# Optimization experiments

Hardware: AMD Instinct MI355X
Metric: run time of the kernel (lower is better)

Reference implementation:

```python
import jax, jax.numpy as jnp
import numpy as np

N_LINK, N_FLOW, N_PATH = 2000, 30000, 50000
E1, E2 = 120000, 120000
HID, H, D = 256, 4, 256  # hidden_size, num_heads, per-head out_feats (= hidden)
OUT = 2
NEG_SLOPE = 0.2


def gat_conv(z_src, z_dst, src, dst, attn_l, attn_r, n_dst, ee=None):
    """Edge-GAT aggregation. z_src:[Ns,H,D], z_dst:[Nd,H,D], ee:[E,H] or None -> [Nd,H,D]."""
    el = (z_src * attn_l).sum(-1)  # [Ns,H]
    er = (z_dst * attn_r).sum(-1)  # [Nd,H]
    e = el[src] + er[dst]          # [E,H]
    if ee is not None:
        e = e + ee
    e = jax.nn.leaky_relu(e, NEG_SLOPE)
    m = jax.ops.segment_max(e, dst, num_segments=n_dst)
    m = jnp.where(jnp.isfinite(m), m, 0.0)  # empty segments -> -inf
    a = jnp.exp(e - m[dst])
    denom = jax.ops.segment_sum(a, dst, num_segments=n_dst)
    alpha = a / jnp.maximum(denom[dst], 1e-9)
    return jax.ops.segment_sum(alpha[:, :, None] * z_src[src], dst, num_segments=n_dst)


def setup_inputs() -> dict:
    key = jax.random.key(0)
    ks = jax.random.split(key, 32)
    s = jnp.float32(0.05)
    lin = lambda k, i, o: (jax.random.normal(k, (i, o), jnp.float32) * s)
    vec = lambda k, h, d: (jax.random.normal(k, (h, d), jnp.float32) * s)
    inp = {
        'x_link': jax.random.normal(ks[0], (N_LINK, 8), jnp.float32),
        'x_flow': jax.random.normal(ks[1], (N_FLOW, 16), jnp.float32),
        'x_path': jax.random.normal(ks[2], (N_PATH, 8), jnp.float32),
        'e2p_feature': jax.random.uniform(ks[3], (E1, 1), jnp.float32),
        'Wp_link': lin(ks[8], 8, HID), 'bp_link': jnp.zeros((HID,), jnp.float32),
        'Wp_flow': lin(ks[9], 16, HID), 'bp_flow': jnp.zeros((HID,), jnp.float32),
        'Wp_path': lin(ks[10], 8, HID), 'bp_path': jnp.zeros((HID,), jnp.float32),
        'fc_src1': lin(ks[11], HID, H * D), 'fc_dst1': lin(ks[12], HID, H * D),
        'fc_e1': lin(ks[13], 1, H * D),
        'attn_l1': vec(ks[14], H, D), 'attn_r1': vec(ks[15], H, D), 'attn_e1': vec(ks[16], H, D),
        'res_W1': lin(ks[17], HID, HID),
        'fc_src2': lin(ks[18], HID, H * D), 'fc_dst2': lin(ks[19], HID, H * D),
        'attn_l2': vec(ks[20], H, D), 'attn_r2': vec(ks[21], H, D),
        'res_W2': lin(ks[22], HID, HID),
        'W1': lin(ks[23], 3 * HID, HID), 'b1': jnp.zeros((HID,), jnp.float32),
        'W2': lin(ks[24], HID, OUT), 'b2': jnp.zeros((OUT,), jnp.float32),
        'src1': jax.random.randint(ks[4], (E1,), 0, N_LINK),
        'dst1': jax.random.randint(ks[5], (E1,), 0, N_PATH),
        'src2': jax.random.randint(ks[6], (E2,), 0, N_FLOW),
        'dst2': jax.random.randint(ks[7], (E2,), 0, N_PATH),
    }
    return inp


def reference(x_link, x_flow, x_path, e2p_feature,
              Wp_link, bp_link, Wp_flow, bp_flow, Wp_path, bp_path,
              fc_src1, fc_dst1, fc_e1, attn_l1, attn_r1, attn_e1, res_W1,
              fc_src2, fc_dst2, attn_l2, attn_r2, res_W2,
              W1, b1, W2, b2, src1, dst1, src2, dst2):
    # per-node-type projection + relu
    h_link = jax.nn.relu(x_link @ Wp_link + bp_link)
    h_flow = jax.nn.relu(x_flow @ Wp_flow + bp_flow)
    h_path = jax.nn.relu(x_path @ Wp_path + bp_path)

    # conv_1: link -> path (edge features e2p_feature, edge_feats=1)
    z_s = (h_link @ fc_src1).reshape(-1, H, D)
    z_d = (h_path @ fc_dst1).reshape(-1, H, D)
    ee = ((e2p_feature @ fc_e1).reshape(-1, H, D) * attn_e1).sum(-1)  # [E1,H]
    agg = gat_conv(z_s, z_d, src1, dst1, attn_l1, attn_r1, N_PATH, ee)
    h_path = jax.nn.relu(agg.mean(axis=1) + h_path @ res_W1)
    x_res1 = h_path

    # conv_2: flow -> path (no edge features)
    z_s = (h_flow @ fc_src2).reshape(-1, H, D)
    z_d = (h_path @ fc_dst2).reshape(-1, H, D)
    agg = gat_conv(z_s, z_d, src2, dst2, attn_l2, attn_r2, N_PATH)
    h_path = jax.nn.relu(agg.mean(axis=1) + h_path @ res_W2)
    x_res2 = h_path

    # linear decoder (dropout = identity in eval)
    x = jnp.concatenate([h_path, x_res1, x_res2], axis=-1)  # [N_PATH, 3*HID]
    x = jax.nn.relu(x @ W1 + b1)
    return x @ W2 + b2  # [N_PATH, OUT]
```

## Files before the change

kernel.cpp:

```cpp
#include <hip/hip_runtime.h>
#include <math.h>

typedef unsigned int uint;
typedef unsigned short ushort;

#define HIDF 256
#define HD4 1024
#define NHEAD 4
#define N_LINK 2000
#define N_FLOW 30000
#define N_PATH 50000
#define NEDGE 120000
#define N_CVT 26
#define NB_SCAN ((N_PATH + 1023) / 1024)

__device__ inline float bf_lo(uint u) { return __uint_as_float(u << 16); }
__device__ inline float bf_hi(uint u) { return __uint_as_float(u & 0xffff0000u); }
__device__ inline float ldb(const ushort* p) { return __uint_as_float(((uint)*p) << 16); }
__device__ inline ushort f2b(float f) {
    uint x = __float_as_uint(f);
    return (ushort)((x + 0x7fffu + ((x >> 16) & 1u)) >> 16);
}

typedef __attribute__((ext_vector_type(8))) short bf16x8;
typedef __attribute__((ext_vector_type(4))) float f32x4;

__global__ void detect_dtype(const ushort* __restrict__ probe, int* __restrict__ flag) {
    int lane = threadIdx.x;
    uint u = probe[lane * 2];
    int e = (u >> 7) & 0xFF;
    bool sane = (u != 0u) && (e <= 0x4F);
    unsigned long long m = __ballot(sane);
    if (lane == 0) *flag = (__popcll(m) >= 48) ? 1 : 0;
}

struct CvtArgs {
    const void* src[N_CVT];
    int off[N_CVT];
    int sz[N_CVT];
};

__global__ __launch_bounds__(256) void convert_inputs(CvtArgs a, ushort* __restrict__ dst,
                                                      const int* __restrict__ flag) {
    int i = blockIdx.y;
    int idx = blockIdx.x * 256 + threadIdx.x;
    if (idx >= a.sz[i]) return;
    ushort v;
    if (*flag) v = ((const ushort*)a.src[i])[idx];
    else       v = f2b(((const float*)a.src[i])[idx]);
    dst[a.off[i] + idx] = v;
}

__global__ void sentinel_fill(void* out, int n, float val, const int* flag) {
    int i = blockIdx.x * 256 + threadIdx.x;
    if (i >= n) return;
    if (*flag) ((ushort*)out)[i] = f2b(val);
    else       ((float*)out)[i] = val;
}

__global__ void prep_small(const ushort* __restrict__ fc_src1, const ushort* __restrict__ attn_l1,
                           const ushort* __restrict__ fc_dst1, const ushort* __restrict__ attn_r1,
                           const ushort* __restrict__ fc_src2, const ushort* __restrict__ attn_l2,
                           const ushort* __restrict__ fc_dst2, const ushort* __restrict__ attn_r2,
                           const ushort* __restrict__ fc_e1,   const ushort* __restrict__ attn_e1,
                           float* wl1, float* wr1, float* wl2, float* wr2, float* c1) {
    int h = blockIdx.x;
    int k = threadIdx.x;
    float a = 0.f, b = 0.f, c = 0.f, d = 0.f;
    for (int dd = 0; dd < HIDF; ++dd) {
        int fi = k * HD4 + h * HIDF + dd;
        int ai = h * HIDF + dd;
        a += ldb(fc_src1 + fi) * ldb(attn_l1 + ai);
        b += ldb(fc_dst1 + fi) * ldb(attn_r1 + ai);
        c += ldb(fc_src2 + fi) * ldb(attn_l2 + ai);
        d += ldb(fc_dst2 + fi) * ldb(attn_r2 + ai);
    }
    wl1[k * NHEAD + h] = a;
    wr1[k * NHEAD + h] = b;
    wl2[k * NHEAD + h] = c;
    wr2[k * NHEAD + h] = d;
    if (k == 0) {
        float s = 0.f;
        for (int dd = 0; dd < HIDF; ++dd) s += ldb(fc_e1 + h * HIDF + dd) * ldb(attn_e1 + h * HIDF + dd);
        c1[h] = s;
    }
}

struct TJobs {
    const ushort* s1[6];
    const ushort* s2[6];
    ushort* d[6];
    int K[6];
    int N[6];
};

__global__ __launch_bounds__(256) void transpose_batch(TJobs tj) {
    int j = blockIdx.y;
    int K = tj.K[j], N = tj.N[j];
    int tilesx = N >> 5;
    if ((int)blockIdx.x >= tilesx * (K >> 5)) return;
    int n0 = (blockIdx.x % tilesx) * 32, k0 = (blockIdx.x / tilesx) * 32;
    const ushort* s1 = tj.s1[j];
    const ushort* s2 = tj.s2[j];
    ushort* dst = tj.d[j];
    __shared__ ushort tile[32][33];
    int jj = threadIdx.x & 31, i0 = threadIdx.x >> 5;
    for (int i = i0; i < 32; i += 8) {
        size_t idx = (size_t)(k0 + i) * N + n0 + jj;
        float v = ldb(s1 + idx);
        if (s2) v += ldb(s2 + idx);
        tile[i][jj] = f2b(v);
    }
    __syncthreads();
    for (int i = i0; i < 32; i += 8) dst[(size_t)(n0 + i) * K + k0 + jj] = tile[jj][i];
}

template <int K>
__device__ inline void proj_body(const ushort* __restrict__ X, const ushort* __restrict__ W,
                                 const ushort* __restrict__ bias, ushort* __restrict__ Y, int i) {
    int j = threadIdx.x;
    float x[K];
#pragma unroll
    for (int k = 0; k < K; ++k) x[k] = ldb(X + i * K + k);
    float s = ldb(bias + j);
#pragma unroll
    for (int k = 0; k < K; ++k) s += x[k] * ldb(W + k * HIDF + j);
    Y[(size_t)i * HIDF + j] = f2b(fmaxf(s, 0.f));
}

__global__ __launch_bounds__(256) void proj_all(const ushort* X0, const ushort* W0, const ushort* b0, ushort* Y0,
                                                const ushort* X1, const ushort* W1, const ushort* b1, ushort* Y1,
                                                const ushort* X2, const ushort* W2, const ushort* b2, ushort* Y2) {
    int b = blockIdx.x;
    if (b < N_LINK) proj_body<8>(X0, W0, b0, Y0, b);
    else if (b < N_LINK + N_FLOW) proj_body<16>(X1, W1, b1, Y1, b - N_LINK);
    else proj_body<8>(X2, W2, b2, Y2, b - N_LINK - N_FLOW);
}

#define GTM 64
#define GTN 128
#define GTK 32
#define GPAD 40

#define LOAD_TILE(t)                                                          \
    {                                                                         \
        const ushort* A;                                                      \
        const ushort* BT;                                                     \
        int K, k0;                                                            \
        if ((t) < nt1) { A = A1; BT = B1T; K = K1; k0 = (t)*GTK; }            \
        else           { A = A2; BT = B2T; K = K2; k0 = ((t)-nt1) * GTK; }    \
        av = (bm + ar < M) ? *(const uint4*)(A + (size_t)(bm + ar) * K + k0 + aq * 8) : z4; \
        bv0 = *(const uint4*)(BT + (size_t)(bn + ar) * K + k0 + aq * 8);      \
        bv1 = *(const uint4*)(BT + (size_t)(bn + ar + 64) * K + k0 + aq * 8); \
    }

#define STORE_TILE(b)                                                         \
    {                                                                         \
        *(uint4*)&As[b][ar][aq * 8] = av;                                     \
        *(uint4*)&Bs[b][ar][aq * 8] = bv0;                                    \
        *(uint4*)&Bs[b][ar + 64][aq * 8] = bv1;                               \
    }

__global__ __launch_bounds__(256) void gemm_mfma(const ushort* __restrict__ A1, const ushort* __restrict__ B1T, int K1,
                                                 const ushort* __restrict__ A2, const ushort* __restrict__ B2T, int K2,
                                                 const ushort* __restrict__ Dadd, const ushort* __restrict__ bias,
                                                 int do_relu, ushort* __restrict__ C, int M, int N) {
    __shared__ __align__(16) ushort As[2][GTM][GPAD];
    __shared__ __align__(16) ushort Bs[2][GTN][GPAD];

    int tid = threadIdx.x;
    int lane = tid & 63, wave = tid >> 6;
    int quad = lane >> 4, l16 = lane & 15;
    int wn = wave * 32;
    int bm = blockIdx.y * GTM, bn = blockIdx.x * GTN;

    f32x4 acc[4][2];
    f32x4 zf = {0.f, 0.f, 0.f, 0.f};
#pragma unroll
    for (int i = 0; i < 4; ++i) {
        acc[i][0] = zf;
        acc[i][1] = zf;
    }

    int ar = tid >> 2, aq = tid & 3;
    uint4 av, bv0, bv1;
    uint4 z4 = {0, 0, 0, 0};

    int nt1 = K1 / GTK;
    int ntot = nt1 + K2 / GTK;

    LOAD_TILE(0);
    STORE_TILE(0);
    __syncthreads();

    for (int t = 0; t < ntot; ++t) {
        int cur = t & 1, nxt = cur ^ 1;
        if (t + 1 < ntot) LOAD_TILE(t + 1);

        bf16x8 af[4], bf[2];
#pragma unroll
        for (int mt = 0; mt < 4; ++mt) af[mt] = *(const bf16x8*)&As[cur][mt * 16 + l16][quad * 8];
#pragma unroll
        for (int ct = 0; ct < 2; ++ct) bf[ct] = *(const bf16x8*)&Bs[cur][wn + ct * 16 + l16][quad * 8];
#pragma unroll
        for (int mt = 0; mt < 4; ++mt)
#pragma unroll
            for (int ct = 0; ct < 2; ++ct)
                acc[mt][ct] = __builtin_amdgcn_mfma_f32_16x16x32_bf16(af[mt], bf[ct], acc[mt][ct], 0, 0, 0);

        if (t + 1 < ntot) STORE_TILE(nxt);
        __syncthreads();
    }

#pragma unroll
    for (int mt = 0; mt < 4; ++mt) {
#pragma unroll
        for (int ct = 0; ct < 2; ++ct) {
            int col = bn + wn + ct * 16 + l16;
#pragma unroll
            for (int rg = 0; rg < 4; ++rg) {
                int row = bm + mt * 16 + quad * 4 + rg;
                if (row >= M) continue;
                float v = acc[mt][ct][rg];
                if (Dadd) v += ldb(Dadd + (size_t)row * N + col);
                if (bias) v += ldb(bias + col);
                if (do_relu) v = fmaxf(v, 0.f);
                C[(size_t)row * N + col] = f2b(v);
            }
        }
    }
}

__device__ inline void rowdot4_body(const ushort* __restrict__ X, const float* __restrict__ W,
                                    float* __restrict__ Y, int row) {
    int lane = threadIdx.x & 63;
    uint2 xu = *(const uint2*)(X + (size_t)row * HIDF + lane * 4);
    float x[4] = {bf_lo(xu.x), bf_hi(xu.x), bf_lo(xu.y), bf_hi(xu.y)};
    float p0 = 0.f, p1 = 0.f, p2 = 0.f, p3 = 0.f;
#pragma unroll
    for (int i = 0; i < 4; ++i) {
        int k = lane * 4 + i;
        p0 += x[i] * W[k * 4 + 0];
        p1 += x[i] * W[k * 4 + 1];
        p2 += x[i] * W[k * 4 + 2];
        p3 += x[i] * W[k * 4 + 3];
    }
#pragma unroll
    for (int off = 32; off >= 1; off >>= 1) {
        p0 += __shfl_down(p0, off, 64);
        p1 += __shfl_down(p1, off, 64);
        p2 += __shfl_down(p2, off, 64);
        p3 += __shfl_down(p3, off, 64);
    }
    if (lane == 0) {
        Y[(size_t)row * 4 + 0] = p0;
        Y[(size_t)row * 4 + 1] = p1;
        Y[(size_t)row * 4 + 2] = p2;
        Y[(size_t)row * 4 + 3] = p3;
    }
}

__global__ __launch_bounds__(256) void rowdot_pair(const ushort* XA, const float* WA, float* YA, int MA,
                                                   const ushort* XB, const float* WB, float* YB, int MB) {
    int nblkA = (MA + 3) / 4;
    int wv = threadIdx.x >> 6;
    if ((int)blockIdx.x < nblkA) {
        int row = blockIdx.x * 4 + wv;
        if (row < MA) rowdot4_body(XA, WA, YA, row);
    } else {
        int row = (blockIdx.x - nblkA) * 4 + wv;
        if (row < MB) rowdot4_body(XB, WB, YB, row);
    }
}

__global__ __launch_bounds__(256) void rowdot_out(const ushort* __restrict__ X, const ushort* __restrict__ W2,
                                                  const ushort* __restrict__ b2, void* __restrict__ Y, int M,
                                                  const int* __restrict__ flag) {
    int wv = threadIdx.x >> 6, lane = threadIdx.x & 63;
    int row = blockIdx.x * 4 + wv;
    if (row >= M) return;
    uint2 xu = *(const uint2*)(X + (size_t)row * HIDF + lane * 4);
    float x[4] = {bf_lo(xu.x), bf_hi(xu.x), bf_lo(xu.y), bf_hi(xu.y)};
    float p0 = 0.f, p1 = 0.f;
#pragma unroll
    for (int i = 0; i < 4; ++i) {
        int k = lane * 4 + i;
        p0 += x[i] * ldb(W2 + k * 2 + 0);
        p1 += x[i] * ldb(W2 + k * 2 + 1);
    }
#pragma unroll
    for (int off = 32; off >= 1; off >>= 1) {
        p0 += __shfl_down(p0, off, 64);
        p1 += __shfl_down(p1, off, 64);
    }
    if (lane == 0) {
        float v0 = p0 + ldb(b2 + 0);
        float v1 = p1 + ldb(b2 + 1);
        if (*flag) {
            ((ushort*)Y)[(size_t)row * 2 + 0] = f2b(v0);
            ((ushort*)Y)[(size_t)row * 2 + 1] = f2b(v1);
        } else {
            ((float*)Y)[(size_t)row * 2 + 0] = v0;
            ((float*)Y)[(size_t)row * 2 + 1] = v1;
        }
    }
}

__global__ void edge_pass_a(const int* __restrict__ src, const int* __restrict__ dst,
                            const float* __restrict__ el, const float* __restrict__ er,
                            const ushort* __restrict__ e2p, const float* __restrict__ c1,
                            float* __restrict__ abuf, float* __restrict__ denom,
                            int* __restrict__ cnt, int E) {
    int e = blockIdx.x * 256 + threadIdx.x;
    if (e >= E) return;
    int s = src[e], d = dst[e];
    float ev = e2p ? ldb(e2p + e) : 0.f;
#pragma unroll
    for (int h = 0; h < NHEAD; ++h) {
        float v = el[s * NHEAD + h] + er[d * NHEAD + h];
        if (e2p) v += c1[h] * ev;
        v = v > 0.f ? v : 0.2f * v;
        float a = __expf(v);
        abuf[e * NHEAD + h] = a;
        atomicAdd(&denom[d * NHEAD + h], a);
    }
    atomicAdd(&cnt[d], 1);
}

__global__ __launch_bounds__(1024) void scan_block(const int* __restrict__ cnt, int* __restrict__ starts,
                                                   int* __restrict__ bsum, int n) {
    __shared__ int sd[1024];
    int t = threadIdx.x, i = blockIdx.x * 1024 + t;
    int x = (i < n) ? cnt[i] : 0;
    sd[t] = x;
    __syncthreads();
    for (int o = 1; o < 1024; o <<= 1) {
        int v = (t >= o) ? sd[t - o] : 0;
        __syncthreads();
        sd[t] += v;
        __syncthreads();
    }
    if (i < n) starts[i] = sd[t] - x;
    if (t == 1023) bsum[blockIdx.x] = sd[t];
}

__global__ void scan_part(int* __restrict__ bsum, int nb) {
    int b = threadIdx.x;
    int x = (b < nb) ? bsum[b] : 0;
    int orig = x;
    for (int o = 1; o < 64; o <<= 1) {
        int v = __shfl_up(x, o, 64);
        if (b >= o) x += v;
    }
    if (b < nb) bsum[b] = x - orig;
}

__global__ __launch_bounds__(1024) void scan_add(int* __restrict__ starts, const int* __restrict__ bsum,
                                                 int n, int total) {
    int i = blockIdx.x * 1024 + threadIdx.x;
    if (i < n) starts[i] += bsum[blockIdx.x];
    if (i == 0) starts[n] = total;
}

__global__ void scatter_w(const int* __restrict__ src, const int* __restrict__ dst,
                          const int* __restrict__ starts, int* __restrict__ fill,
                          const float* __restrict__ abuf, const float* __restrict__ denom,
                          int* __restrict__ ssrc, float4* __restrict__ sal, int E) {
    int e = blockIdx.x * 256 + threadIdx.x;
    if (e >= E) return;
    int d = dst[e];
    int p = starts[d] + atomicAdd(&fill[d], 1);
    ssrc[p] = src[e];
    float4 v;
    v.x = abuf[e * 4 + 0] * (0.25f / fmaxf(denom[d * 4 + 0], 1e-9f));
    v.y = abuf[e * 4 + 1] * (0.25f / fmaxf(denom[d * 4 + 1], 1e-9f));
    v.z = abuf[e * 4 + 2] * (0.25f / fmaxf(denom[d * 4 + 2], 1e-9f));
    v.w = abuf[e * 4 + 3] * (0.25f / fmaxf(denom[d * 4 + 3], 1e-9f));
    sal[p] = v;
}

__global__ __launch_bounds__(256) void gather_agg(const int* __restrict__ ssrc, const float* __restrict__ sal,
                                                  const int* __restrict__ starts, const ushort* __restrict__ zs,
                                                  ushort* __restrict__ aggb, int r0, int r1, int first) {
    __shared__ float sh[4][256];
    int d = blockIdx.x;
    int w = threadIdx.x >> 6, l = threadIdx.x & 63;
    int s0 = starts[d], s1 = starts[d + 1];
    float a0 = 0.f, a1 = 0.f, a2 = 0.f, a3 = 0.f;
    const ushort* zcol = zs + w * 256 + l * 4;
    for (int i = s0; i < s1; ++i) {
        int s = ssrc[i];
        if (s < r0 || s >= r1) continue;
        float al = sal[i * 4 + w];
        uint2 zv = *(const uint2*)(zcol + (size_t)(s - r0) * HD4);
        a0 += al * bf_lo(zv.x);
        a1 += al * bf_hi(zv.x);
        a2 += al * bf_lo(zv.y);
        a3 += al * bf_hi(zv.y);
    }
    sh[w][l * 4 + 0] = a0;
    sh[w][l * 4 + 1] = a1;
    sh[w][l * 4 + 2] = a2;
    sh[w][l * 4 + 3] = a3;
    __syncthreads();
    int t = threadIdx.x;
    float tot = sh[0][t] + sh[1][t] + sh[2][t] + sh[3][t];
    size_t oi = (size_t)d * HIDF + t;
    if (!first) tot += ldb(aggb + oi);
    aggb[oi] = f2b(tot);
}

extern "C" void kernel_launch(void* const* d_in, const int* in_sizes, int n_in,
                              void* d_out, int out_size, void* d_ws, size_t ws_size,
                              hipStream_t stream) {
    const int* src1 = (const int*)d_in[26];
    const int* dst1 = (const int*)d_in[27];
    const int* src2 = (const int*)d_in[28];
    const int* dst2 = (const int*)d_in[29];

    static const int csz[N_CVT] = {
        N_LINK * 8, N_FLOW * 16, N_PATH * 8, NEDGE,
        8 * 256, 256, 16 * 256, 256, 8 * 256, 256,
        256 * 1024, 256 * 1024, 1024, 1024, 1024, 1024,
        256 * 256, 256 * 1024, 256 * 1024, 1024, 1024, 256 * 256,
        768 * 256, 256, 256 * 2, 2};

    char* base = (char*)d_ws;
    size_t off = 0;
    auto alloc = [&](size_t bytes) { size_t r = off; off += (bytes + 255) & ~255ull; return r; };

    size_t o_flag = alloc(256);
    CvtArgs ca;
    int coff[N_CVT];
    {
        int acc = 0;
        for (int i = 0; i < N_CVT; ++i) {
            ca.src[i] = d_in[i];
            ca.sz[i] = csz[i];
            ca.off[i] = acc;
            coff[i] = acc;
            acc += (csz[i] + 127) & ~127;
        }
        alloc((size_t)acc * 2);
    }
    const ushort* cvt = (const ushort*)(base + o_flag + 256);
    auto IN = [&](int i) { return cvt + coff[i]; };

    size_t o_h_link  = alloc((size_t)N_LINK * HIDF * 2);
    size_t o_h_flow  = alloc((size_t)N_FLOW * HIDF * 2);
    size_t o_h_path0 = alloc((size_t)N_PATH * HIDF * 2);
    size_t o_h1      = alloc((size_t)N_PATH * HIDF * 2);
    size_t o_h2      = alloc((size_t)N_PATH * HIDF * 2);
    size_t o_aggb    = alloc((size_t)N_PATH * HIDF * 2);
    size_t o_el      = alloc((size_t)N_FLOW * NHEAD * 4);
    size_t o_er      = alloc((size_t)N_PATH * NHEAD * 4);
    size_t o_abuf    = alloc((size_t)NEDGE * NHEAD * 4);
    size_t o_denom   = alloc((size_t)N_PATH * NHEAD * 4);
    size_t o_cnt     = alloc((size_t)(N_PATH + 1) * 4);
    size_t o_fill    = alloc((size_t)(N_PATH + 1) * 4);
    size_t zero_span = o_fill + (size_t)(N_PATH + 1) * 4 - o_denom;
    size_t o_wl1 = alloc(HIDF * NHEAD * 4);
    size_t o_wr1 = alloc(HIDF * NHEAD * 4);
    size_t o_wl2 = alloc(HIDF * NHEAD * 4);
    size_t o_wr2 = alloc(HIDF * NHEAD * 4);
    size_t o_c1  = alloc(NHEAD * 4);
    size_t o_bt_src1 = alloc((size_t)HD4 * HIDF * 2);
    size_t o_bt_src2 = alloc((size_t)HD4 * HIDF * 2);
    size_t o_bt_rw1  = alloc((size_t)HIDF * HIDF * 2);
    size_t o_bt_rw2  = alloc((size_t)HIDF * HIDF * 2);
    size_t o_bt_w1ac = alloc((size_t)HIDF * HIDF * 2);
    size_t o_bt_w1b  = alloc((size_t)HIDF * HIDF * 2);
    size_t o_starts = alloc((size_t)(N_PATH + 2) * 4);
    size_t o_ssrc   = alloc((size_t)NEDGE * 4);
    size_t o_sal    = alloc((size_t)NEDGE * 16);
    size_t o_bsum   = alloc(64 * 4);
    size_t o_zs = off;

    int* flag = (int*)(base + o_flag);

    long avail = (long)ws_size - (long)off;
    long Rl = avail / (HD4 * 2);
    int R = (int)(Rl > N_FLOW ? N_FLOW : Rl);
    R &= ~63;
    detect_dtype<<<1, 64, 0, stream>>>((const ushort*)d_in[13], flag);
    if (R < 256) {
        sentinel_fill<<<(out_size + 255) / 256, 256, 0, stream>>>(d_out, out_size,
                                                                  (float)(ws_size >> 20), flag);
        return;
    }

    ushort* h_link = (ushort*)(base + o_h_link);
    ushort* h_flow = (ushort*)(base + o_h_flow);
    ushort* h_path0 = (ushort*)(base + o_h_path0);
    ushort* h1 = (ushort*)(base + o_h1);
    ushort* h2 = (ushort*)(base + o_h2);
    ushort* zs = (ushort*)(base + o_zs);
    ushort* aggb = (ushort*)(base + o_aggb);
    float* el = (float*)(base + o_el);
    float* er = (float*)(base + o_er);
    float* abuf = (float*)(base + o_abuf);
    float* denom = (float*)(base + o_denom);
    int* cnt = (int*)(base + o_cnt);
    int* fill = (int*)(base + o_fill);
    float* wl1 = (float*)(base + o_wl1);
    float* wr1 = (float*)(base + o_wr1);
    float* wl2 = (float*)(base + o_wl2);
    float* wr2 = (float*)(base + o_wr2);
    float* c1 = (float*)(base + o_c1);
    ushort* bt_src1 = (ushort*)(base + o_bt_src1);
    ushort* bt_src2 = (ushort*)(base + o_bt_src2);
    ushort* bt_rw1 = (ushort*)(base + o_bt_rw1);
    ushort* bt_rw2 = (ushort*)(base + o_bt_rw2);
    ushort* bt_w1ac = (ushort*)(base + o_bt_w1ac);
    ushort* bt_w1b = (ushort*)(base + o_bt_w1b);
    int* starts = (int*)(base + o_starts);
    int* ssrc = (int*)(base + o_ssrc);
    float* sal = (float*)(base + o_sal);
    int* bsum = (int*)(base + o_bsum);

    convert_inputs<<<dim3((N_FLOW * 16 + 255) / 256, N_CVT), 256, 0, stream>>>(
        ca, (ushort*)(base + o_flag + 256), flag);

    ushort* hidden = h_path0;

    prep_small<<<NHEAD, 256, 0, stream>>>(IN(10), IN(13), IN(11), IN(14),
                                          IN(17), IN(19), IN(18), IN(20),
                                          IN(12), IN(15), wl1, wr1, wl2, wr2, c1);
    TJobs tj;
    tj.s1[0] = IN(10); tj.s2[0] = nullptr;            tj.d[0] = bt_src1; tj.K[0] = HIDF; tj.N[0] = HD4;
    tj.s1[1] = IN(17); tj.s2[1] = nullptr;            tj.d[1] = bt_src2; tj.K[1] = HIDF; tj.N[1] = HD4;
    tj.s1[2] = IN(16); tj.s2[2] = nullptr;            tj.d[2] = bt_rw1;  tj.K[2] = HIDF; tj.N[2] = HIDF;
    tj.s1[3] = IN(21); tj.s2[3] = nullptr;            tj.d[3] = bt_rw2;  tj.K[3] = HIDF; tj.N[3] = HIDF;
    tj.s1[4] = IN(22); tj.s2[4] = IN(22) + 512 * 256; tj.d[4] = bt_w1ac; tj.K[4] = HIDF; tj.N[4] = HIDF;
    tj.s1[5] = IN(22) + 256 * 256; tj.s2[5] = nullptr; tj.d[5] = bt_w1b; tj.K[5] = HIDF; tj.N[5] = HIDF;
    transpose_batch<<<dim3(256, 6), 256, 0, stream>>>(tj);

    proj_all<<<N_LINK + N_FLOW + N_PATH, 256, 0, stream>>>(
        IN(0), IN(4), IN(5), h_link, IN(1), IN(6), IN(7), h_flow, IN(2), IN(8), IN(9), h_path0);

    const int EB = (NEDGE + 255) / 256;

    hipMemsetAsync(denom, 0, zero_span, stream);
    rowdot_pair<<<(N_LINK + 3) / 4 + (N_PATH + 3) / 4, 256, 0, stream>>>(
        h_link, wl1, el, N_LINK, h_path0, wr1, er, N_PATH);
    edge_pass_a<<<EB, 256, 0, stream>>>(src1, dst1, el, er, IN(3), c1, abuf, denom, cnt, NEDGE);
    scan_block<<<NB_SCAN, 1024, 0, stream>>>(cnt, starts, bsum, N_PATH);
    scan_part<<<1, 64, 0, stream>>>(bsum, NB_SCAN);
    scan_add<<<NB_SCAN, 1024, 0, stream>>>(starts, bsum, N_PATH, NEDGE);
    scatter_w<<<EB, 256, 0, stream>>>(src1, dst1, starts, fill, abuf, denom, ssrc, (float4*)sal, NEDGE);
    for (int r0 = 0; r0 < N_LINK; r0 += R) {
        int r1 = r0 + R < N_LINK ? r0 + R : N_LINK;
        gemm_mfma<<<dim3(HD4 / GTN, (r1 - r0 + GTM - 1) / GTM), 256, 0, stream>>>(
            h_link + (size_t)r0 * HIDF, bt_src1, HIDF, nullptr, nullptr, 0,
            nullptr, nullptr, 0, zs, r1 - r0, HD4);
        gather_agg<<<N_PATH, 256, 0, stream>>>(ssrc, sal, starts, zs, aggb, r0, r1, r0 == 0);
    }
    gemm_mfma<<<dim3(HIDF / GTN, (N_PATH + GTM - 1) / GTM), 256, 0, stream>>>(
        h_path0, bt_rw1, HIDF, nullptr, nullptr, 0, aggb, nullptr, 1, h1, N_PATH, HIDF);

    hipMemsetAsync(denom, 0, zero_span, stream);
    rowdot_pair<<<(N_FLOW + 3) / 4 + (N_PATH + 3) / 4, 256, 0, stream>>>(
        h_flow, wl2, el, N_FLOW, h1, wr2, er, N_PATH);
    edge_pass_a<<<EB, 256, 0, stream>>>(src2, dst2, el, er, nullptr, nullptr, abuf, denom, cnt, NEDGE);
    scan_block<<<NB_SCAN, 1024, 0, stream>>>(cnt, starts, bsum, N_PATH);
    scan_part<<<1, 64, 0, stream>>>(bsum, NB_SCAN);
    scan_add<<<NB_SCAN, 1024, 0, stream>>>(starts, bsum, N_PATH, NEDGE);
    scatter_w<<<EB, 256, 0, stream>>>(src2, dst2, starts, fill, abuf, denom, ssrc, (float4*)sal, NEDGE);
    for (int r0 = 0; r0 < N_FLOW; r0 += R) {
        int r1 = r0 + R < N_FLOW ? r0 + R : N_FLOW;
        gemm_mfma<<<dim3(HD4 / GTN, (r1 - r0 + GTM - 1) / GTM), 256, 0, stream>>>(
            h_flow + (size_t)r0 * HIDF, bt_src2, HIDF, nullptr, nullptr, 0,
            nullptr, nullptr, 0, zs, r1 - r0, HD4);
        gather_agg<<<N_PATH, 256, 0, stream>>>(ssrc, sal, starts, zs, aggb, r0, r1, r0 == 0);
    }
    gemm_mfma<<<dim3(HIDF / GTN, (N_PATH + GTM - 1) / GTM), 256, 0, stream>>>(
        h1, bt_rw2, HIDF, nullptr, nullptr, 0, aggb, nullptr, 1, h2, N_PATH, HIDF);

    gemm_mfma<<<dim3(HIDF / GTN, (N_PATH + GTM - 1) / GTM), 256, 0, stream>>>(
        h2, bt_w1ac, HIDF, h1, bt_w1b, HIDF, nullptr, IN(23), 1, hidden, N_PATH, HIDF);
    rowdot_out<<<(N_PATH + 3) / 4, 256, 0, stream>>>(hidden, IN(24), IN(25), d_out, N_PATH, flag);
}
```

Before: 687.8 us.

## Build both CSR graphs once upfront and gather with one wave per node

Builds the destination-sorted CSR for both edge sets in a single combined histogram, scan and scatter pass at the start, in place of a separate build per conv layer. The scatter now stores (src, edge id), and gather_agg computes the normalized attention from abuf and denom on the fly. Each wave handles one destination node with 16-wide bf16 loads per lane and a prefetched next edge, so the shared-memory reduction and sync go away. Separate denominator buffers are kept per layer, at the cost of extra indirection through abuf inside the gather loop.

```diff
diff --git a/kernel.cpp b/kernel.cpp
--- a/kernel.cpp
+++ b/kernel.cpp
@@ -12,7 +12,9 @@
 #define N_PATH 50000
 #define NEDGE 120000
 #define N_CVT 26
-#define NB_SCAN ((N_PATH + 1023) / 1024)
+#define NPP (N_PATH + 1)
+#define NSCAN (2 * NPP)
+#define NB2 ((NSCAN + 1023) / 1024)
 
 __device__ inline float bf_lo(uint u) { return __uint_as_float(u << 16); }
 __device__ inline float bf_hi(uint u) { return __uint_as_float(u & 0xffff0000u); }
@@ -309,8 +311,7 @@
 __global__ void edge_pass_a(const int* __restrict__ src, const int* __restrict__ dst,
                             const float* __restrict__ el, const float* __restrict__ er,
                             const ushort* __restrict__ e2p, const float* __restrict__ c1,
-                            float* __restrict__ abuf, float* __restrict__ denom,
-                            int* __restrict__ cnt, int E) {
+                            float* __restrict__ abuf, float* __restrict__ denom, int E) {
     int e = blockIdx.x * 256 + threadIdx.x;
     if (e >= E) return;
     int s = src[e], d = dst[e];
@@ -324,7 +325,14 @@
         abuf[e * NHEAD + h] = a;
         atomicAdd(&denom[d * NHEAD + h], a);
     }
-    atomicAdd(&cnt[d], 1);
+}
+
+__global__ void hist2_kernel(const int* __restrict__ dst1, const int* __restrict__ dst2,
+                             int* __restrict__ cnt, int E) {
+    int e = blockIdx.x * 256 + threadIdx.x;
+    if (e >= E) return;
+    atomicAdd(&cnt[dst1[e]], 1);
+    atomicAdd(&cnt[NPP + dst2[e]], 1);
 }
 
 __global__ __launch_bounds__(1024) void scan_block(const int* __restrict__ cnt, int* __restrict__ starts,
@@ -344,70 +352,106 @@
     if (t == 1023) bsum[blockIdx.x] = sd[t];
 }
 
-__global__ void scan_part(int* __restrict__ bsum, int nb) {
-    int b = threadIdx.x;
-    int x = (b < nb) ? bsum[b] : 0;
-    int orig = x;
-    for (int o = 1; o < 64; o <<= 1) {
-        int v = __shfl_up(x, o, 64);
-        if (b >= o) x += v;
-    }
-    if (b < nb) bsum[b] = x - orig;
-}
-
-__global__ __launch_bounds__(1024) void scan_add(int* __restrict__ starts, const int* __restrict__ bsum,
-                                                 int n, int total) {
+__global__ __launch_bounds__(1024) void scan_small(int* __restrict__ bsum, int nb) {
+    __shared__ int sd[1024];
+    int t = threadIdx.x;
+    int x = (t < nb) ? bsum[t] : 0;
+    sd[t] = x;
+    __syncthreads();
+    for (int o = 1; o < 1024; o <<= 1) {
+        int v = (t >= o) ? sd[t - o] : 0;
+        __syncthreads();
+        sd[t] += v;
+        __syncthreads();
+    }
+    if (t < nb) bsum[t] = sd[t] - x;
+}
+
+__global__ __launch_bounds__(1024) void scan_add(int* __restrict__ starts, const int* __restrict__ bsum, int n) {
     int i = blockIdx.x * 1024 + threadIdx.x;
     if (i < n) starts[i] += bsum[blockIdx.x];
-    if (i == 0) starts[n] = total;
-}
-
-__global__ void scatter_w(const int* __restrict__ src, const int* __restrict__ dst,
-                          const int* __restrict__ starts, int* __restrict__ fill,
-                          const float* __restrict__ abuf, const float* __restrict__ denom,
-                          int* __restrict__ ssrc, float4* __restrict__ sal, int E) {
+}
+
+__global__ void scatter2_kernel(const int* __restrict__ src1, const int* __restrict__ dst1,
+                                const int* __restrict__ src2, const int* __restrict__ dst2,
+                                const int* __restrict__ starts, int* __restrict__ fill,
+                                int2* __restrict__ seg, int E) {
     int e = blockIdx.x * 256 + threadIdx.x;
     if (e >= E) return;
-    int d = dst[e];
+    int d = dst1[e];
     int p = starts[d] + atomicAdd(&fill[d], 1);
-    ssrc[p] = src[e];
-    float4 v;
-    v.x = abuf[e * 4 + 0] * (0.25f / fmaxf(denom[d * 4 + 0], 1e-9f));
-    v.y = abuf[e * 4 + 1] * (0.25f / fmaxf(denom[d * 4 + 1], 1e-9f));
-    v.z = abuf[e * 4 + 2] * (0.25f / fmaxf(denom[d * 4 + 2], 1e-9f));
-    v.w = abuf[e * 4 + 3] * (0.25f / fmaxf(denom[d * 4 + 3], 1e-9f));
-    sal[p] = v;
-}
-
-__global__ __launch_bounds__(256) void gather_agg(const int* __restrict__ ssrc, const float* __restrict__ sal,
-                                                  const int* __restrict__ starts, const ushort* __restrict__ zs,
-                                                  ushort* __restrict__ aggb, int r0, int r1, int first) {
-    __shared__ float sh[4][256];
-    int d = blockIdx.x;
-    int w = threadIdx.x >> 6, l = threadIdx.x & 63;
+    seg[p] = make_int2(src1[e], e);
+    int d2 = NPP + dst2[e];
+    int p2 = starts[d2] + atomicAdd(&fill[d2], 1);
+    seg[p2] = make_int2(src2[e], e);
+}
+
+__global__ __launch_bounds__(256) void gather_agg(const int2* __restrict__ seg, const int* __restrict__ starts,
+                                                  const float4* __restrict__ abufv, const float4* __restrict__ denomv,
+                                                  const ushort* __restrict__ zs, ushort* __restrict__ aggb,
+                                                  int r0, int r1, int first) {
+    int wave = threadIdx.x >> 6, lane = threadIdx.x & 63;
+    int d = blockIdx.x * 4 + wave;
+    int h = lane >> 4;
+    int c16 = (lane & 15) * 16;
     int s0 = starts[d], s1 = starts[d + 1];
-    float a0 = 0.f, a1 = 0.f, a2 = 0.f, a3 = 0.f;
-    const ushort* zcol = zs + w * 256 + l * 4;
+    float4 dn = denomv[d];
+    float rd = 0.25f / fmaxf(h == 0 ? dn.x : h == 1 ? dn.y : h == 2 ? dn.z : dn.w, 1e-9f);
+    float acc[16];
+#pragma unroll
+    for (int j = 0; j < 16; ++j) acc[j] = 0.f;
+
+    int2 se = make_int2(0, 0);
+    if (s0 < s1) se = seg[s0];
     for (int i = s0; i < s1; ++i) {
-        int s = ssrc[i];
-        if (s < r0 || s >= r1) continue;
-        float al = sal[i * 4 + w];
-        uint2 zv = *(const uint2*)(zcol + (size_t)(s - r0) * HD4);
-        a0 += al * bf_lo(zv.x);
-        a1 += al * bf_hi(zv.x);
-        a2 += al * bf_lo(zv.y);
-        a3 += al * bf_hi(zv.y);
-    }
-    sh[w][l * 4 + 0] = a0;
-    sh[w][l * 4 + 1] = a1;
-    sh[w][l * 4 + 2] = a2;
-    sh[w][l * 4 + 3] = a3;
-    __syncthreads();
-    int t = threadIdx.x;
-    float tot = sh[0][t] + sh[1][t] + sh[2][t] + sh[3][t];
-    size_t oi = (size_t)d * HIDF + t;
-    if (!first) tot += ldb(aggb + oi);
-    aggb[oi] = f2b(tot);
+        int2 nse = se;
+        if (i + 1 < s1) nse = seg[i + 1];
+        int s = se.x;
+        if (s >= r0 && s < r1) {
+            float4 av = abufv[se.y];
+            float al = (h == 0 ? av.x : h == 1 ? av.y : h == 2 ? av.z : av.w) * rd;
+            const ushort* zr = zs + (size_t)(s - r0) * HD4 + h * 256 + c16;
+            uint4 z0 = *(const uint4*)zr;
+            uint4 z1 = *(const uint4*)(zr + 8);
+            acc[0] += al * bf_lo(z0.x);  acc[1] += al * bf_hi(z0.x);
+            acc[2] += al * bf_lo(z0.y);  acc[3] += al * bf_hi(z0.y);
+            acc[4] += al * bf_lo(z0.z);  acc[5] += al * bf_hi(z0.z);
+            acc[6] += al * bf_lo(z0.w);  acc[7] += al * bf_hi(z0.w);
+            acc[8] += al * bf_lo(z1.x);  acc[9] += al * bf_hi(z1.x);
+            acc[10] += al * bf_lo(z1.y); acc[11] += al * bf_hi(z1.y);
+            acc[12] += al * bf_lo(z1.z); acc[13] += al * bf_hi(z1.z);
+            acc[14] += al * bf_lo(z1.w); acc[15] += al * bf_hi(z1.w);
+        }
+        se = nse;
+    }
+
+#pragma unroll
+    for (int j = 0; j < 16; ++j) {
+        acc[j] += __shfl_xor(acc[j], 16, 64);
+        acc[j] += __shfl_xor(acc[j], 32, 64);
+    }
+
+    if (h == 0) {
+        size_t oi = (size_t)d * HIDF + c16;
+        if (!first) {
+            uint4 p0 = *(const uint4*)(aggb + oi);
+            uint4 p1 = *(const uint4*)(aggb + oi + 8);
+            acc[0] += bf_lo(p0.x);  acc[1] += bf_hi(p0.x);
+            acc[2] += bf_lo(p0.y);  acc[3] += bf_hi(p0.y);
+            acc[4] += bf_lo(p0.z);  acc[5] += bf_hi(p0.z);
+            acc[6] += bf_lo(p0.w);  acc[7] += bf_hi(p0.w);
+            acc[8] += bf_lo(p1.x);  acc[9] += bf_hi(p1.x);
+            acc[10] += bf_lo(p1.y); acc[11] += bf_hi(p1.y);
+            acc[12] += bf_lo(p1.z); acc[13] += bf_hi(p1.z);
+            acc[14] += bf_lo(p1.w); acc[15] += bf_hi(p1.w);
+        }
+        uint uo[8];
+#pragma unroll
+        for (int j = 0; j < 8; ++j)
+            uo[j] = (uint)f2b(acc[2 * j]) | ((uint)f2b(acc[2 * j + 1]) << 16);
+        *(uint4*)(aggb + oi) = make_uint4(uo[0], uo[1], uo[2], uo[3]);
+        *(uint4*)(aggb + oi + 8) = make_uint4(uo[4], uo[5], uo[6], uo[7]);
+    }
 }
 
 extern "C" void kernel_launch(void* const* d_in, const int* in_sizes, int n_in,
@@ -455,10 +499,11 @@
     size_t o_el      = alloc((size_t)N_FLOW * NHEAD * 4);
     size_t o_er      = alloc((size_t)N_PATH * NHEAD * 4);
     size_t o_abuf    = alloc((size_t)NEDGE * NHEAD * 4);
-    size_t o_denom   = alloc((size_t)N_PATH * NHEAD * 4);
-    size_t o_cnt     = alloc((size_t)(N_PATH + 1) * 4);
-    size_t o_fill    = alloc((size_t)(N_PATH + 1) * 4);
-    size_t zero_span = o_fill + (size_t)(N_PATH + 1) * 4 - o_denom;
+    size_t o_denom1  = alloc((size_t)N_PATH * NHEAD * 4);
+    size_t o_denom2  = alloc((size_t)N_PATH * NHEAD * 4);
+    size_t o_cnt     = alloc((size_t)NSCAN * 4);
+    size_t o_fill    = alloc((size_t)NSCAN * 4);
+    size_t zero_span = o_fill + (size_t)NSCAN * 4 - o_denom1;
     size_t o_wl1 = alloc(HIDF * NHEAD * 4);
     size_t o_wr1 = alloc(HIDF * NHEAD * 4);
     size_t o_wl2 = alloc(HIDF * NHEAD * 4);
@@ -470,10 +515,9 @@
     size_t o_bt_rw2  = alloc((size_t)HIDF * HIDF * 2);
     size_t o_bt_w1ac = alloc((size_t)HIDF * HIDF * 2);
     size_t o_bt_w1b  = alloc((size_t)HIDF * HIDF * 2);
-    size_t o_starts = alloc((size_t)(N_PATH + 2) * 4);
-    size_t o_ssrc   = alloc((size_t)NEDGE * 4);
-    size_t o_sal    = alloc((size_t)NEDGE * 16);
-    size_t o_bsum   = alloc(64 * 4);
+    size_t o_starts = alloc((size_t)(NSCAN + 1) * 4);
+    size_t o_seg    = alloc((size_t)(2 * NEDGE) * 8);
+    size_t o_bsum   = alloc(1024 * 4);
     size_t o_zs = off;
 
     int* flag = (int*)(base + o_flag);
@@ -499,7 +543,8 @@
     float* el = (float*)(base + o_el);
     float* er = (float*)(base + o_er);
     float* abuf = (float*)(base + o_abuf);
-    float* denom = (float*)(base + o_denom);
+    float* denom1 = (float*)(base + o_denom1);
+    float* denom2 = (float*)(base + o_denom2);
     int* cnt = (int*)(base + o_cnt);
     int* fill = (int*)(base + o_fill);
     float* wl1 = (float*)(base + o_wl1);
@@ -514,15 +559,20 @@
     ushort* bt_w1ac = (ushort*)(base + o_bt_w1ac);
     ushort* bt_w1b = (ushort*)(base + o_bt_w1b);
     int* starts = (int*)(base + o_starts);
-    int* ssrc = (int*)(base + o_ssrc);
-    float* sal = (float*)(base + o_sal);
+    int2* seg = (int2*)(base + o_seg);
     int* bsum = (int*)(base + o_bsum);
+
+    const int EB = (NEDGE + 255) / 256;
+
+    hipMemsetAsync(denom1, 0, zero_span, stream);
+    hist2_kernel<<<EB, 256, 0, stream>>>(dst1, dst2, cnt, NEDGE);
+    scan_block<<<NB2, 1024, 0, stream>>>(cnt, starts, bsum, NSCAN);
+    scan_small<<<1, 1024, 0, stream>>>(bsum, NB2);
+    scan_add<<<NB2, 1024, 0, stream>>>(starts, bsum, NSCAN);
+    scatter2_kernel<<<EB, 256, 0, stream>>>(src1, dst1, src2, dst2, starts, fill, seg, NEDGE);
 
     convert_inputs<<<dim3((N_FLOW * 16 + 255) / 256, N_CVT), 256, 0, stream>>>(
         ca, (ushort*)(base + o_flag + 256), flag);
-
-    ushort* hidden = h_path0;
-
     prep_small<<<NHEAD, 256, 0, stream>>>(IN(10), IN(13), IN(11), IN(14),
                                           IN(17), IN(19), IN(18), IN(20),
                                           IN(12), IN(15), wl1, wr1, wl2, wr2, c1);
@@ -538,40 +588,32 @@
     proj_all<<<N_LINK + N_FLOW + N_PATH, 256, 0, stream>>>(
         IN(0), IN(4), IN(5), h_link, IN(1), IN(6), IN(7), h_flow, IN(2), IN(8), IN(9), h_path0);
 
-    const int EB = (NEDGE + 255) / 256;
-
-    hipMemsetAsync(denom, 0, zero_span, stream);
+    ushort* hidden = h_path0;
+
     rowdot_pair<<<(N_LINK + 3) / 4 + (N_PATH + 3) / 4, 256, 0, stream>>>(
         h_link, wl1, el, N_LINK, h_path0, wr1, er, N_PATH);
-    edge_pass_a<<<EB, 256, 0, stream>>>(src1, dst1, el, er, IN(3), c1, abuf, denom, cnt, NEDGE);
-    scan_block<<<NB_SCAN, 1024, 0, stream>>>(cnt, starts, bsum, N_PATH);
-    scan_part<<<1, 64, 0, stream>>>(bsum, NB_SCAN);
-    scan_add<<<NB_SCAN, 1024, 0, stream>>>(starts, bsum, N_PATH, NEDGE);
-    scatter_w<<<EB, 256, 0, stream>>>(src1, dst1, starts, fill, abuf, denom, ssrc, (float4*)sal, NEDGE);
+    edge_pass_a<<<EB, 256, 0, stream>>>(src1, dst1, el, er, IN(3), c1, abuf, denom1, NEDGE);
     for (int r0 = 0; r0 < N_LINK; r0 += R) {
         int r1 = r0 + R < N_LINK ? r0 + R : N_LINK;
         gemm_mfma<<<dim3(HD4 / GTN, (r1 - r0 + GTM - 1) / GTM), 256, 0, stream>>>(
             h_link + (size_t)r0 * HIDF, bt_src1, HIDF, nullptr, nullptr, 0,
             nullptr, nullptr, 0, zs, r1 - r0, HD4);
-        gather_agg<<<N_PATH, 256, 0, stream>>>(ssrc, sal, starts, zs, aggb, r0, r1, r0 == 0);
+        gather_agg<<<N_PATH / 4, 256, 0, stream>>>(seg, starts, (const float4*)abuf, (const float4*)denom1,
+                                                   zs, aggb, r0, r1, r0 == 0);
     }
     gemm_mfma<<<dim3(HIDF / GTN, (N_PATH + GTM - 1) / GTM), 256, 0, stream>>>(
         h_path0, bt_rw1, HIDF, nullptr, nullptr, 0, aggb, nullptr, 1, h1, N_PATH, HIDF);
 
-    hipMemsetAsync(denom, 0, zero_span, stream);
     rowdot_pair<<<(N_FLOW + 3) / 4 + (N_PATH + 3) / 4, 256, 0, stream>>>(
         h_flow, wl2, el, N_FLOW, h1, wr2, er, N_PATH);
-    edge_pass_a<<<EB, 256, 0, stream>>>(src2, dst2, el, er, nullptr, nullptr, abuf, denom, cnt, NEDGE);
-    scan_block<<<NB_SCAN, 1024, 0, stream>>>(cnt, starts, bsum, N_PATH);
-    scan_part<<<1, 64, 0, stream>>>(bsum, NB_SCAN);
-    scan_add<<<NB_SCAN, 1024, 0, stream>>>(starts, bsum, N_PATH, NEDGE);
-    scatter_w<<<EB, 256, 0, stream>>>(src2, dst2, starts, fill, abuf, denom, ssrc, (float4*)sal, NEDGE);
+    edge_pass_a<<<EB, 256, 0, stream>>>(src2, dst2, el, er, nullptr, nullptr, abuf, denom2, NEDGE);
     for (int r0 = 0; r0 < N_FLOW; r0 += R) {
         int r1 = r0 + R < N_FLOW ? r0 + R : N_FLOW;
         gemm_mfma<<<dim3(HD4 / GTN, (r1 - r0 + GTM - 1) / GTM), 256, 0, stream>>>(
             h_flow + (size_t)r0 * HIDF, bt_src2, HIDF, nullptr, nullptr, 0,
             nullptr, nullptr, 0, zs, r1 - r0, HD4);
-        gather_agg<<<N_PATH, 256, 0, stream>>>(ssrc, sal, starts, zs, aggb, r0, r1, r0 == 0);
+        gather_agg<<<N_PATH / 4, 256, 0, stream>>>(seg, starts + NPP, (const float4*)abuf, (const float4*)denom2,
+                                                   zs, aggb, r0, r1, r0 == 0);
     }
     gemm_mfma<<<dim3(HIDF / GTN, (N_PATH + GTM - 1) / GTM), 256, 0, stream>>>(
         h1, bt_rw2, HIDF, nullptr, nullptr, 0, aggb, nullptr, 1, h2, N_PATH, HIDF);
```

Measured after the change: 639.8 us. 1.07x faster.
